# Kernel tuning notes

Measured on AMD Instinct MI355X. Metric: run time of the kernel, lower is better.

## Reference

```python
import jax, jax.numpy as jnp
import numpy as np

EPS_NORM = 1e-12  # F.normalize eps
BN_EPS = 1e-5     # BatchNorm2d eps
N_NODES = 18
T_STEPS = 1280
FC_IN = 1469952


def _temporal_conv(x, wa, ba, wb, bb, wc, bc):
    """Gated temporal conv (GLU) from STConv's TemporalConv.
    x: (B, T, N, C) -> (B, T-k+1, N, Cout)."""
    xp = jnp.transpose(x, (0, 3, 2, 1))  # (B, C, N, T)

    def conv(w, b):
        y = jax.lax.conv_general_dilated(
            xp, w, window_strides=(1, 1), padding='VALID',
            dimension_numbers=('NCHW', 'OIHW', 'NCHW'))
        return y + b[None, :, None, None]

    P = conv(wa, ba)
    Q = jax.nn.sigmoid(conv(wb, bb))
    H = jax.nn.relu(P * Q + conv(wc, bc))
    return jnp.transpose(H, (0, 3, 2, 1))  # (B, T', N, Cout)


def setup_inputs() -> dict:
    key = jax.random.key(0)
    ks = jax.random.split(key, 16)
    s = 0.05
    inp = {
        'x': jax.random.normal(ks[0], (N_NODES, 1, T_STEPS), dtype=jnp.float32),
        'edge_index': jax.random.randint(ks[1], (2, 306), 0, N_NODES, dtype=jnp.int64),
        'edge_weight': jax.random.uniform(ks[2], (306,), dtype=jnp.float32),
        'w1a': jax.random.normal(ks[3], (64, 1, 1, 3), dtype=jnp.float32) * s,
        'b1a': jnp.zeros((64,), jnp.float32),
        'w1b': jax.random.normal(ks[4], (64, 1, 1, 3), dtype=jnp.float32) * s,
        'b1b': jnp.zeros((64,), jnp.float32),
        'w1c': jax.random.normal(ks[5], (64, 1, 1, 3), dtype=jnp.float32) * s,
        'b1c': jnp.zeros((64,), jnp.float32),
        'cheb_w': jax.random.normal(ks[6], (64, 64), dtype=jnp.float32) * s,
        'cheb_b': jnp.zeros((64,), jnp.float32),
        'w2a': jax.random.normal(ks[7], (64, 64, 1, 3), dtype=jnp.float32) * s,
        'b2a': jnp.zeros((64,), jnp.float32),
        'w2b': jax.random.normal(ks[8], (64, 64, 1, 3), dtype=jnp.float32) * s,
        'b2b': jnp.zeros((64,), jnp.float32),
        'w2c': jax.random.normal(ks[9], (64, 64, 1, 3), dtype=jnp.float32) * s,
        'b2c': jnp.zeros((64,), jnp.float32),
        'bn_gamma': jnp.ones((N_NODES,), jnp.float32),
        'bn_beta': jnp.zeros((N_NODES,), jnp.float32),
        'fc_w': jax.random.normal(ks[10], (1, FC_IN), dtype=jnp.float32) * 0.001,
        'fc_b': jnp.zeros((1,), jnp.float32),
    }
    return inp


def reference(x, edge_index, edge_weight,
              w1a, b1a, w1b, b1b, w1c, b1c,
              cheb_w, cheb_b,
              w2a, b2a, w2b, b2b, w2c, b2c,
              bn_gamma, bn_beta, fc_w, fc_b):
    # F.normalize(x, dim=1): x shape (N, 1, T)
    norm = jnp.sqrt(jnp.sum(x * x, axis=1, keepdims=True))
    xn = x / jnp.maximum(norm, EPS_NORM)
    # x[None].reshape([1, shape[3], shape[1], shape[2]]): row-major reshape (faithful)
    X = jnp.reshape(xn[None], (1, xn.shape[2], xn.shape[0], xn.shape[1]))  # (1, T, N, 1)

    T0 = _temporal_conv(X, w1a, b1a, w1b, b1b, w1c, b1c)  # (1, T-2, N, 64)
    # ChebConv with K=1: only T_0 = I term -> per-node linear; edge_index/edge_weight unused
    T = jnp.einsum('btnc,cd->btnd', T0, cheb_w) + cheb_b
    T = jax.nn.relu(T)
    T = _temporal_conv(T, w2a, b2a, w2b, b2b, w2c, b2c)  # (1, T-4, N, 64)

    # BatchNorm2d(num_nodes) in training mode: normalize per-node over (B, T, C)
    Tp = jnp.transpose(T, (0, 2, 1, 3))  # (B, N, T, C)
    mean = jnp.mean(Tp, axis=(0, 2, 3), keepdims=True)
    var = jnp.mean((Tp - mean) ** 2, axis=(0, 2, 3), keepdims=True)  # biased var
    Tn = (Tp - mean) / jnp.sqrt(var + BN_EPS)
    Tn = Tn * bn_gamma[None, :, None, None] + bn_beta[None, :, None, None]
    h = jnp.transpose(Tn, (0, 2, 1, 3))  # (B, T-4, N, C)

    h = jax.nn.relu(h).reshape(-1)  # flatten(start_dim=0)
    return fc_w @ h + fc_b  # (1,)
```

## Files before the change

kernel.cpp:

```cpp
#include <hip/hip_runtime.h>
#include <math.h>

#define NN 18
#define T_STEPS 1280
#define T1LEN 1278
#define T2LEN 1276
#define PREPBLK 144
#define TC2 92
#define NCHUNK2 ((T2LEN + TC2 - 1) / TC2)
#define NBLK (NCHUNK2 * NN)
#define DOT_BLOCKS 512

typedef __attribute__((ext_vector_type(8))) short short8;
typedef __attribute__((ext_vector_type(4))) float f32x4;

__device__ __forceinline__ unsigned short f2bf(float v) {
    unsigned u = __builtin_bit_cast(unsigned, v);
    u = u + 0x7fff + ((u >> 16) & 1);
    return (unsigned short)(u >> 16);
}
__device__ __forceinline__ float bf2f(unsigned short h) {
    unsigned u = ((unsigned)h) << 16;
    return __builtin_bit_cast(float, u);
}
__device__ __forceinline__ int swz(int row, int c) {
    return row * 64 + (((c >> 3) ^ (row & 7)) << 3) + (c & 7);
}

__global__ void k_wprep(const float* __restrict__ wa, const float* __restrict__ wb,
                        const float* __restrict__ wc,
                        unsigned short* __restrict__ WBhi, unsigned short* __restrict__ WBlo) {
    int i = blockIdx.x * 256 + threadIdx.x;
    if (i >= 6 * 192 * 32) return;
    int klocal = i & 31;
    int col = (i >> 5) % 192;
    int kb = i / (192 * 32);
    int conv = col >> 6, co = col & 63;
    int k = kb >> 1, ci = (kb & 1) * 32 + klocal;
    const float* w = (conv == 0) ? wa : (conv == 1 ? wb : wc);
    float v = w[co * 192 + ci * 3 + k];
    unsigned short hi = f2bf(v);
    WBhi[i] = hi;
    WBlo[i] = f2bf(v - bf2f(hi));
}

__global__ __launch_bounds__(256) void k_fuseall(const float* __restrict__ x,
        const float* __restrict__ w1a, const float* __restrict__ b1a,
        const float* __restrict__ w1b, const float* __restrict__ b1b,
        const float* __restrict__ w1c, const float* __restrict__ b1c,
        const float* __restrict__ cw, const float* __restrict__ cb,
        const unsigned short* __restrict__ WBhi, const unsigned short* __restrict__ WBlo,
        const float* __restrict__ b2a, const float* __restrict__ b2b,
        const float* __restrict__ b2c,
        float* __restrict__ T2, float* __restrict__ parts) {
    __shared__ float xs[104];
    __shared__ uint4 t1H[768], t1L[768];
    __shared__ uint4 t2H[784], t2L[784];
    __shared__ float red1[256], red2[256];
    int b = blockIdx.x;
    int node = b / NCHUNK2, chunk = b % NCHUNK2;
    int t0 = chunk * TC2;
    int tid = threadIdx.x;
    int l = tid & 63, w = tid >> 6;

    if (tid < 98) {
        int xt = t0 + tid;
        float v = (xt < T_STEPS) ? x[xt * NN + node] : 0.f;
        xs[tid] = v / fmaxf(fabsf(v), 1e-12f);
    }
    __syncthreads();

    {
        unsigned short* tH = (unsigned short*)t1H;
        unsigned short* tL = (unsigned short*)t1L;
        int c = l;
        float wa0 = w1a[c*3], wa1 = w1a[c*3+1], wa2 = w1a[c*3+2];
        float wb0 = w1b[c*3], wb1 = w1b[c*3+1], wb2 = w1b[c*3+2];
        float wc0 = w1c[c*3], wc1 = w1c[c*3+1], wc2 = w1c[c*3+2];
        float ba = b1a[c], bb = b1b[c], bc = b1c[c];
        #pragma unroll
        for (int j = 0; j < 24; ++j) {
            int r = w * 24 + j;
            float x0 = xs[r], x1 = xs[r + 1], x2 = xs[r + 2];
            float pa = fmaf(wa2, x2, fmaf(wa1, x1, fmaf(wa0, x0, ba)));
            float pb = fmaf(wb2, x2, fmaf(wb1, x1, fmaf(wb0, x0, bb)));
            float pc_ = fmaf(wc2, x2, fmaf(wc1, x1, fmaf(wc0, x0, bc)));
            float q = 1.0f / (1.0f + expf(-pb));
            float v = fmaxf(pa * q + pc_, 0.f);
            if (t0 + r >= T1LEN) v = 0.f;
            unsigned short hi = f2bf(v);
            int sw = swz(r, c);
            tH[sw] = hi;
            tL[sw] = f2bf(v - bf2f(hi));
        }
    }
    int d = w * 16 + (l & 15);
    short8 cbh[2], cbl[2];
    #pragma unroll
    for (int kb = 0; kb < 2; ++kb) {
        #pragma unroll
        for (int j = 0; j < 8; ++j) {
            float v = cw[(kb * 32 + (l >> 4) * 8 + j) * 64 + d];
            unsigned short hi = f2bf(v);
            cbh[kb][j] = (short)hi;
            cbl[kb][j] = (short)f2bf(v - bf2f(hi));
        }
    }
    __syncthreads();
    {
        f32x4 acc1[6];
        #pragma unroll
        for (int mt = 0; mt < 6; ++mt) acc1[mt] = (f32x4){0.f,0.f,0.f,0.f};
        #pragma unroll
        for (int kb = 0; kb < 2; ++kb) {
            #pragma unroll
            for (int mt = 0; mt < 6; ++mt) {
                int row = mt * 16 + (l & 15);
                int cbi = kb * 4 + (l >> 4);
                int si = row * 8 + (cbi ^ (row & 7));
                short8 ah = __builtin_bit_cast(short8, t1H[si]);
                short8 al = __builtin_bit_cast(short8, t1L[si]);
                acc1[mt] = __builtin_amdgcn_mfma_f32_16x16x32_bf16(ah, cbh[kb], acc1[mt], 0, 0, 0);
                acc1[mt] = __builtin_amdgcn_mfma_f32_16x16x32_bf16(al, cbh[kb], acc1[mt], 0, 0, 0);
                acc1[mt] = __builtin_amdgcn_mfma_f32_16x16x32_bf16(ah, cbl[kb], acc1[mt], 0, 0, 0);
            }
        }
        float cbias = cb[d];
        unsigned short* tH = (unsigned short*)t2H;
        unsigned short* tL = (unsigned short*)t2L;
        #pragma unroll
        for (int mt = 0; mt < 6; ++mt) {
            #pragma unroll
            for (int r = 0; r < 4; ++r) {
                int row = mt * 16 + (l >> 4) * 4 + r;
                float v = fmaxf(acc1[mt][r] + cbias, 0.f);
                if (t0 + row >= T1LEN) v = 0.f;
                unsigned short hi = f2bf(v);
                int sw = swz(row, d);
                tH[sw] = hi;
                tL[sw] = f2bf(v - bf2f(hi));
            }
        }
        if (tid < 128) {
            int row = 96 + (tid >> 6), c = tid & 63;
            int sw = swz(row, c);
            tH[sw] = 0; tL[sw] = 0;
        }
    }
    __syncthreads();
    float s_sum = 0.f, s_sq = 0.f;
    {
        const uint4* wbh = (const uint4*)WBhi;
        const uint4* wbl = (const uint4*)WBlo;
        int co = w * 16 + (l & 15);
        f32x4 acc[6][3];
        #pragma unroll
        for (int mt = 0; mt < 6; ++mt)
            #pragma unroll
            for (int ct = 0; ct < 3; ++ct)
                acc[mt][ct] = (f32x4){0.f, 0.f, 0.f, 0.f};
        for (int kb = 0; kb < 6; ++kb) {
            short8 bh[3], bl[3];
            #pragma unroll
            for (int ct = 0; ct < 3; ++ct) {
                int col = (w + 4 * ct) * 16 + (l & 15);
                int gi = (kb * 192 + col) * 4 + (l >> 4);
                bh[ct] = __builtin_bit_cast(short8, wbh[gi]);
                bl[ct] = __builtin_bit_cast(short8, wbl[gi]);
            }
            #pragma unroll
            for (int mt = 0; mt < 6; ++mt) {
                int row = mt * 16 + (l & 15) + (kb >> 1);
                int cb2 = (kb & 1) * 4 + (l >> 4);
                int si = row * 8 + (cb2 ^ (row & 7));
                short8 ah = __builtin_bit_cast(short8, t2H[si]);
                short8 al = __builtin_bit_cast(short8, t2L[si]);
                acc[mt][0] = __builtin_amdgcn_mfma_f32_16x16x32_bf16(ah, bh[0], acc[mt][0], 0, 0, 0);
                acc[mt][1] = __builtin_amdgcn_mfma_f32_16x16x32_bf16(ah, bh[1], acc[mt][1], 0, 0, 0);
                acc[mt][2] = __builtin_amdgcn_mfma_f32_16x16x32_bf16(ah, bh[2], acc[mt][2], 0, 0, 0);
                acc[mt][0] = __builtin_amdgcn_mfma_f32_16x16x32_bf16(al, bh[0], acc[mt][0], 0, 0, 0);
                acc[mt][1] = __builtin_amdgcn_mfma_f32_16x16x32_bf16(al, bh[1], acc[mt][1], 0, 0, 0);
                acc[mt][2] = __builtin_amdgcn_mfma_f32_16x16x32_bf16(al, bh[2], acc[mt][2], 0, 0, 0);
                acc[mt][0] = __builtin_amdgcn_mfma_f32_16x16x32_bf16(ah, bl[0], acc[mt][0], 0, 0, 0);
                acc[mt][1] = __builtin_amdgcn_mfma_f32_16x16x32_bf16(ah, bl[1], acc[mt][1], 0, 0, 0);
                acc[mt][2] = __builtin_amdgcn_mfma_f32_16x16x32_bf16(ah, bl[2], acc[mt][2], 0, 0, 0);
            }
        }
        float ba = b2a[co], bb = b2b[co], bc = b2c[co];
        #pragma unroll
        for (int mt = 0; mt < 6; ++mt) {
            #pragma unroll
            for (int r = 0; r < 4; ++r) {
                int tl2 = mt * 16 + (l >> 4) * 4 + r;
                int t = t0 + tl2;
                if (tl2 < TC2 && t < T2LEN) {
                    float P = acc[mt][0][r] + ba, Q = acc[mt][1][r] + bb, Cc = acc[mt][2][r] + bc;
                    float qs = 1.f / (1.f + expf(-Q));
                    float hv = fmaxf(fmaf(P, qs, Cc), 0.f);
                    T2[(t * NN + node) * 64 + co] = hv;
                    s_sum += hv;
                    s_sq = fmaf(hv, hv, s_sq);
                }
            }
        }
    }
    red1[tid] = s_sum; red2[tid] = s_sq;
    __syncthreads();
    for (int off = 128; off > 0; off >>= 1) {
        if (tid < off) { red1[tid] += red1[tid + off]; red2[tid] += red2[tid + off]; }
        __syncthreads();
    }
    if (tid == 0) {
        parts[b * 2]     = red1[0];
        parts[b * 2 + 1] = red2[0];
    }
}

__global__ __launch_bounds__(256) void k_dot2(const float* __restrict__ T2,
        const float* __restrict__ parts,
        const float* __restrict__ gamma, const float* __restrict__ beta,
        const float* __restrict__ fcw, float* __restrict__ dpart) {
    __shared__ float sm[NN * 4];
    if (threadIdx.x < NN) {
        int n = threadIdx.x;
        float s = 0.f, q = 0.f;
        for (int i = 0; i < NCHUNK2; ++i) {
            s += parts[(n * NCHUNK2 + i) * 2];
            q += parts[(n * NCHUNK2 + i) * 2 + 1];
        }
        float cnt = (float)(T2LEN * 64);
        float mean = s / cnt;
        float var = q / cnt - mean * mean;
        sm[n * 4]     = mean;
        sm[n * 4 + 1] = rsqrtf(var + 1e-5f);
        sm[n * 4 + 2] = gamma[n];
        sm[n * 4 + 3] = beta[n];
    }
    __syncthreads();
    float acc = 0.f;
    const int total4 = T2LEN * NN * 64 / 4;
    const float4* T24 = (const float4*)T2;
    const float4* fw4 = (const float4*)fcw;
    for (int i = blockIdx.x * 256 + threadIdx.x; i < total4; i += DOT_BLOCKS * 256) {
        float4 t = T24[i];
        float4 f = fw4[i];
        int n = (i >> 4) % NN;
        float mu = sm[n * 4], is = sm[n * 4 + 1], g = sm[n * 4 + 2], bt = sm[n * 4 + 3];
        float v0 = fmaxf((t.x - mu) * is * g + bt, 0.f);
        float v1 = fmaxf((t.y - mu) * is * g + bt, 0.f);
        float v2 = fmaxf((t.z - mu) * is * g + bt, 0.f);
        float v3 = fmaxf((t.w - mu) * is * g + bt, 0.f);
        acc = fmaf(v0, f.x, acc);
        acc = fmaf(v1, f.y, acc);
        acc = fmaf(v2, f.z, acc);
        acc = fmaf(v3, f.w, acc);
    }
    __shared__ float r[256];
    r[threadIdx.x] = acc;
    __syncthreads();
    for (int off = 128; off > 0; off >>= 1) {
        if (threadIdx.x < off) r[threadIdx.x] += r[threadIdx.x + off];
        __syncthreads();
    }
    if (threadIdx.x == 0) dpart[blockIdx.x] = r[0];
}

__global__ __launch_bounds__(512) void k_final(const float* __restrict__ dpart,
                                               const float* __restrict__ fcb,
                                               float* __restrict__ out) {
    __shared__ float r[512];
    r[threadIdx.x] = dpart[threadIdx.x];
    __syncthreads();
    for (int off = 256; off > 0; off >>= 1) {
        if (threadIdx.x < off) r[threadIdx.x] += r[threadIdx.x + off];
        __syncthreads();
    }
    if (threadIdx.x == 0) out[0] = r[0] + fcb[0];
}

extern "C" void kernel_launch(void* const* d_in, const int* in_sizes, int n_in,
                              void* d_out, int out_size, void* d_ws, size_t ws_size,
                              hipStream_t stream) {
    const float* x     = (const float*)d_in[0];
    const float* w1a   = (const float*)d_in[3];
    const float* b1a   = (const float*)d_in[4];
    const float* w1b   = (const float*)d_in[5];
    const float* b1b   = (const float*)d_in[6];
    const float* w1c   = (const float*)d_in[7];
    const float* b1c   = (const float*)d_in[8];
    const float* chw   = (const float*)d_in[9];
    const float* chb   = (const float*)d_in[10];
    const float* w2a   = (const float*)d_in[11];
    const float* b2a   = (const float*)d_in[12];
    const float* w2b   = (const float*)d_in[13];
    const float* b2b   = (const float*)d_in[14];
    const float* w2c   = (const float*)d_in[15];
    const float* b2c   = (const float*)d_in[16];
    const float* gamma = (const float*)d_in[17];
    const float* beta  = (const float*)d_in[18];
    const float* fcw   = (const float*)d_in[19];
    const float* fcb   = (const float*)d_in[20];
    float* out = (float*)d_out;

    char* base = (char*)d_ws;
    float*          T2v   = (float*)(base);
    unsigned short* WBhi  = (unsigned short*)(base + 5879808);
    unsigned short* WBlo  = (unsigned short*)(base + 5953536);
    float*          parts = (float*)(base + 6027264);
    float*          dpart = (float*)(base + 6030336);

    k_wprep<<<PREPBLK, 256, 0, stream>>>(w2a, w2b, w2c, WBhi, WBlo);
    k_fuseall<<<NBLK, 256, 0, stream>>>(
        x, w1a, b1a, w1b, b1b, w1c, b1c, chw, chb,
        WBhi, WBlo, b2a, b2b, b2c, T2v, parts);
    k_dot2<<<DOT_BLOCKS, 256, 0, stream>>>(T2v, parts, gamma, beta, fcw, dpart);
    k_final<<<1, 512, 0, stream>>>(dpart, fcb, out);
}
```

Before: 30.75 us.

## Fuse BatchNorm, FC dot and final reduction into conv kernel via grid barrier

```diff
diff --git a/kernel.cpp b/kernel.cpp
--- a/kernel.cpp
+++ b/kernel.cpp
@@ -9,7 +9,6 @@
 #define TC2 92
 #define NCHUNK2 ((T2LEN + TC2 - 1) / TC2)
 #define NBLK (NCHUNK2 * NN)
-#define DOT_BLOCKS 512
 
 typedef __attribute__((ext_vector_type(8))) short short8;
 typedef __attribute__((ext_vector_type(4))) float f32x4;
@@ -26,11 +25,19 @@
 __device__ __forceinline__ int swz(int row, int c) {
     return row * 64 + (((c >> 3) ^ (row & 7)) << 3) + (c & 7);
 }
+__device__ __forceinline__ float ratomic_ld(const float* p) {
+    return __hip_atomic_load(p, __ATOMIC_RELAXED, __HIP_MEMORY_SCOPE_AGENT);
+}
+__device__ __forceinline__ void ratomic_st(float* p, float v) {
+    __hip_atomic_store(p, v, __ATOMIC_RELAXED, __HIP_MEMORY_SCOPE_AGENT);
+}
 
 __global__ void k_wprep(const float* __restrict__ wa, const float* __restrict__ wb,
                         const float* __restrict__ wc,
-                        unsigned short* __restrict__ WBhi, unsigned short* __restrict__ WBlo) {
+                        unsigned short* __restrict__ WBhi, unsigned short* __restrict__ WBlo,
+                        int* __restrict__ cnts) {
     int i = blockIdx.x * 256 + threadIdx.x;
+    if (blockIdx.x == 0 && threadIdx.x < 38) cnts[threadIdx.x * 32] = 0;
     if (i >= 6 * 192 * 32) return;
     int klocal = i & 31;
     int col = (i >> 5) % 192;
@@ -44,7 +51,7 @@
     WBlo[i] = f2bf(v - bf2f(hi));
 }
 
-__global__ __launch_bounds__(256) void k_fuseall(const float* __restrict__ x,
+__global__ __launch_bounds__(256) void k_mega(const float* __restrict__ x,
         const float* __restrict__ w1a, const float* __restrict__ b1a,
         const float* __restrict__ w1b, const float* __restrict__ b1b,
         const float* __restrict__ w1c, const float* __restrict__ b1c,
@@ -52,16 +59,25 @@
         const unsigned short* __restrict__ WBhi, const unsigned short* __restrict__ WBlo,
         const float* __restrict__ b2a, const float* __restrict__ b2b,
         const float* __restrict__ b2c,
-        float* __restrict__ T2, float* __restrict__ parts) {
+        const float* __restrict__ gamma, const float* __restrict__ beta,
+        const float* __restrict__ fcw, const float* __restrict__ fcb,
+        float* parts, float* dpart, float* ndot, int* cnts,
+        float* __restrict__ out) {
     __shared__ float xs[104];
     __shared__ uint4 t1H[768], t1L[768];
     __shared__ uint4 t2H[784], t2L[784];
     __shared__ float red1[256], red2[256];
+    __shared__ float pl[2 * NCHUNK2];
+    __shared__ int flagNode, flagAll;
     int b = blockIdx.x;
     int node = b / NCHUNK2, chunk = b % NCHUNK2;
     int t0 = chunk * TC2;
     int tid = threadIdx.x;
     int l = tid & 63, w = tid >> 6;
+    int* cntA = cnts + node * 32;
+    int* cntB = cnts + 18 * 32;
+    int* cntC = cnts + (19 + node) * 32;
+    int* cntD = cnts + 37 * 32;
 
     if (tid < 98) {
         int xt = t0 + tid;
@@ -148,11 +164,12 @@
         }
     }
     __syncthreads();
+    float hval[24];
+    int co = w * 16 + (l & 15);
     float s_sum = 0.f, s_sq = 0.f;
     {
         const uint4* wbh = (const uint4*)WBhi;
         const uint4* wbl = (const uint4*)WBlo;
-        int co = w * 16 + (l & 15);
         f32x4 acc[6][3];
         #pragma unroll
         for (int mt = 0; mt < 6; ++mt)
@@ -193,14 +210,15 @@
             for (int r = 0; r < 4; ++r) {
                 int tl2 = mt * 16 + (l >> 4) * 4 + r;
                 int t = t0 + tl2;
+                float hv = 0.f;
                 if (tl2 < TC2 && t < T2LEN) {
                     float P = acc[mt][0][r] + ba, Q = acc[mt][1][r] + bb, Cc = acc[mt][2][r] + bc;
                     float qs = 1.f / (1.f + expf(-Q));
-                    float hv = fmaxf(fmaf(P, qs, Cc), 0.f);
-                    T2[(t * NN + node) * 64 + co] = hv;
+                    hv = fmaxf(fmaf(P, qs, Cc), 0.f);
                     s_sum += hv;
                     s_sq = fmaf(hv, hv, s_sq);
                 }
+                hval[mt * 4 + r] = hv;
             }
         }
     }
@@ -211,71 +229,80 @@
         __syncthreads();
     }
     if (tid == 0) {
-        parts[b * 2]     = red1[0];
-        parts[b * 2 + 1] = red2[0];
-    }
-}
-
-__global__ __launch_bounds__(256) void k_dot2(const float* __restrict__ T2,
-        const float* __restrict__ parts,
-        const float* __restrict__ gamma, const float* __restrict__ beta,
-        const float* __restrict__ fcw, float* __restrict__ dpart) {
-    __shared__ float sm[NN * 4];
-    if (threadIdx.x < NN) {
-        int n = threadIdx.x;
-        float s = 0.f, q = 0.f;
-        for (int i = 0; i < NCHUNK2; ++i) {
-            s += parts[(n * NCHUNK2 + i) * 2];
-            q += parts[(n * NCHUNK2 + i) * 2 + 1];
-        }
-        float cnt = (float)(T2LEN * 64);
-        float mean = s / cnt;
-        float var = q / cnt - mean * mean;
-        sm[n * 4]     = mean;
-        sm[n * 4 + 1] = rsqrtf(var + 1e-5f);
-        sm[n * 4 + 2] = gamma[n];
-        sm[n * 4 + 3] = beta[n];
-    }
-    __syncthreads();
+        ratomic_st(&parts[b * 2],     red1[0]);
+        ratomic_st(&parts[b * 2 + 1], red2[0]);
+        asm volatile("s_waitcnt vmcnt(0)" ::: "memory");
+        int o = __hip_atomic_fetch_add(cntA, 1, __ATOMIC_RELAXED, __HIP_MEMORY_SCOPE_AGENT);
+        if (o == NCHUNK2 - 1)
+            __hip_atomic_fetch_add(cntB, 1, __ATOMIC_RELAXED, __HIP_MEMORY_SCOPE_AGENT);
+        while (__hip_atomic_load(cntB, __ATOMIC_RELAXED, __HIP_MEMORY_SCOPE_AGENT) < NN)
+            __builtin_amdgcn_s_sleep(8);
+    }
+    __syncthreads();
+    if (tid < 2 * NCHUNK2) pl[tid] = ratomic_ld(&parts[node * 2 * NCHUNK2 + tid]);
+    __syncthreads();
+    float s = 0.f, q = 0.f;
+    #pragma unroll
+    for (int i = 0; i < NCHUNK2; ++i) { s += pl[2 * i]; q += pl[2 * i + 1]; }
+    float cntf = (float)(T2LEN * 64);
+    float mean = s / cntf;
+    float var = q / cntf - mean * mean;
+    float istd = rsqrtf(var + 1e-5f);
+    float g = gamma[node], bt = beta[node];
     float acc = 0.f;
-    const int total4 = T2LEN * NN * 64 / 4;
-    const float4* T24 = (const float4*)T2;
-    const float4* fw4 = (const float4*)fcw;
-    for (int i = blockIdx.x * 256 + threadIdx.x; i < total4; i += DOT_BLOCKS * 256) {
-        float4 t = T24[i];
-        float4 f = fw4[i];
-        int n = (i >> 4) % NN;
-        float mu = sm[n * 4], is = sm[n * 4 + 1], g = sm[n * 4 + 2], bt = sm[n * 4 + 3];
-        float v0 = fmaxf((t.x - mu) * is * g + bt, 0.f);
-        float v1 = fmaxf((t.y - mu) * is * g + bt, 0.f);
-        float v2 = fmaxf((t.z - mu) * is * g + bt, 0.f);
-        float v3 = fmaxf((t.w - mu) * is * g + bt, 0.f);
-        acc = fmaf(v0, f.x, acc);
-        acc = fmaf(v1, f.y, acc);
-        acc = fmaf(v2, f.z, acc);
-        acc = fmaf(v3, f.w, acc);
-    }
-    __shared__ float r[256];
-    r[threadIdx.x] = acc;
+    #pragma unroll
+    for (int mt = 0; mt < 6; ++mt) {
+        #pragma unroll
+        for (int r = 0; r < 4; ++r) {
+            int tl2 = mt * 16 + (l >> 4) * 4 + r;
+            int t = t0 + tl2;
+            if (tl2 < TC2 && t < T2LEN) {
+                float v = fmaxf((hval[mt * 4 + r] - mean) * istd * g + bt, 0.f);
+                acc = fmaf(v, fcw[(t * NN + node) * 64 + co], acc);
+            }
+        }
+    }
+    red1[tid] = acc;
     __syncthreads();
     for (int off = 128; off > 0; off >>= 1) {
-        if (threadIdx.x < off) r[threadIdx.x] += r[threadIdx.x + off];
-        __syncthreads();
-    }
-    if (threadIdx.x == 0) dpart[blockIdx.x] = r[0];
-}
-
-__global__ __launch_bounds__(512) void k_final(const float* __restrict__ dpart,
-                                               const float* __restrict__ fcb,
-                                               float* __restrict__ out) {
-    __shared__ float r[512];
-    r[threadIdx.x] = dpart[threadIdx.x];
-    __syncthreads();
-    for (int off = 256; off > 0; off >>= 1) {
-        if (threadIdx.x < off) r[threadIdx.x] += r[threadIdx.x + off];
-        __syncthreads();
-    }
-    if (threadIdx.x == 0) out[0] = r[0] + fcb[0];
+        if (tid < off) red1[tid] += red1[tid + off];
+        __syncthreads();
+    }
+    if (tid == 0) {
+        ratomic_st(&dpart[b], red1[0]);
+        asm volatile("s_waitcnt vmcnt(0)" ::: "memory");
+        int o = __hip_atomic_fetch_add(cntC, 1, __ATOMIC_RELAXED, __HIP_MEMORY_SCOPE_AGENT);
+        flagNode = (o == NCHUNK2 - 1);
+    }
+    __syncthreads();
+    if (!flagNode) return;
+    {
+        float v = (tid < NCHUNK2) ? ratomic_ld(&dpart[node * NCHUNK2 + tid]) : 0.f;
+        red1[tid] = v;
+        __syncthreads();
+        for (int off = 128; off > 0; off >>= 1) {
+            if (tid < off) red1[tid] += red1[tid + off];
+            __syncthreads();
+        }
+        if (tid == 0) {
+            ratomic_st(&ndot[node], red1[0]);
+            asm volatile("s_waitcnt vmcnt(0)" ::: "memory");
+            int o2 = __hip_atomic_fetch_add(cntD, 1, __ATOMIC_RELAXED, __HIP_MEMORY_SCOPE_AGENT);
+            flagAll = (o2 == NN - 1);
+        }
+        __syncthreads();
+    }
+    if (!flagAll) return;
+    {
+        float v = (tid < NN) ? ratomic_ld(&ndot[tid]) : 0.f;
+        red1[tid] = v;
+        __syncthreads();
+        for (int off = 128; off > 0; off >>= 1) {
+            if (tid < off) red1[tid] += red1[tid + off];
+            __syncthreads();
+        }
+        if (tid == 0) out[0] = red1[0] + fcb[0];
+    }
 }
 
 extern "C" void kernel_launch(void* const* d_in, const int* in_sizes, int n_in,
@@ -303,16 +330,16 @@
     float* out = (float*)d_out;
 
     char* base = (char*)d_ws;
-    float*          T2v   = (float*)(base);
-    unsigned short* WBhi  = (unsigned short*)(base + 5879808);
-    unsigned short* WBlo  = (unsigned short*)(base + 5953536);
-    float*          parts = (float*)(base + 6027264);
-    float*          dpart = (float*)(base + 6030336);
-
-    k_wprep<<<PREPBLK, 256, 0, stream>>>(w2a, w2b, w2c, WBhi, WBlo);
-    k_fuseall<<<NBLK, 256, 0, stream>>>(
+    unsigned short* WBhi  = (unsigned short*)(base);
+    unsigned short* WBlo  = (unsigned short*)(base + 73728);
+    float*          parts = (float*)(base + 147456);
+    float*          dpart = (float*)(base + 149504);
+    float*          ndot  = (float*)(base + 150528);
+    int*            cnts  = (int*)(base + 150656);
+
+    k_wprep<<<PREPBLK, 256, 0, stream>>>(w2a, w2b, w2c, WBhi, WBlo, cnts);
+    k_mega<<<NBLK, 256, 0, stream>>>(
         x, w1a, b1a, w1b, b1b, w1c, b1c, chw, chb,
-        WBhi, WBlo, b2a, b2b, b2c, T2v, parts);
-    k_dot2<<<DOT_BLOCKS, 256, 0, stream>>>(T2v, parts, gamma, beta, fcw, dpart);
-    k_final<<<1, 512, 0, stream>>>(dpart, fcb, out);
-}
+        WBhi, WBlo, b2a, b2b, b2c, gamma, beta, fcw, fcb,
+        parts, dpart, ndot, cnts, out);
+}
```

Result: slower. 32.80 us (+6.7%).
